# Optimization experiments

Measured on AMD Instinct MI355X. Metric: run time of the kernel, lower is better.

## Reference

```python
import jax, jax.numpy as jnp
import numpy as np

N_NODES = 100000
N_EDGES = 800000
D_IN = 128
D_H = 512


def _glorot(key, shape):
    fan_in, fan_out = shape[1], shape[0]
    lim = jnp.sqrt(6.0 / (fan_in + fan_out))
    return jax.random.uniform(key, shape, jnp.float32, -lim, lim)


def setup_inputs() -> dict:
    key = jax.random.key(0)
    ks = jax.random.split(key, 16)
    x = jax.random.normal(ks[0], (N_NODES, D_IN), jnp.float32)
    edge_index = jax.random.randint(ks[1], (2, N_EDGES), 0, N_NODES, jnp.int64)
    return {
        "x": x,
        "edge_index": edge_index,
        # SAGEConv layer1: lin_l (neighbors, with bias), lin_r (root, no bias)
        "Wl1": _glorot(ks[2], (D_H, D_IN)), "bl1": jnp.zeros((D_H,), jnp.float32),
        "Wr1": _glorot(ks[3], (D_H, D_IN)),
        # SAGEConv layer2
        "Wl2": _glorot(ks[4], (D_H, D_H)), "bl2": jnp.zeros((D_H,), jnp.float32),
        "Wr2": _glorot(ks[5], (D_H, D_H)),
        # SAGEConv layer3
        "Wl3": _glorot(ks[6], (D_H, D_H)), "bl3": jnp.zeros((D_H,), jnp.float32),
        "Wr3": _glorot(ks[7], (D_H, D_H)),
        # residual projections W, W2 (nn.Linear with bias)
        "Ww": _glorot(ks[8], (D_H, D_IN)), "bw": jnp.zeros((D_H,), jnp.float32),
        "Ww2": _glorot(ks[9], (D_H, D_IN)), "bw2": jnp.zeros((D_H,), jnp.float32),
        # shared PReLU parameter (nn.PReLU default: single param init 0.25)
        "a": jnp.array(0.25, jnp.float32),
    }


def _prelu(x, a):
    return jnp.where(x > 0, x, a * x)


def _sage_conv(x, src, dst, Wl, bl, Wr):
    # mean-aggregate neighbor features x[src] onto dst, then linear + root term
    msg = jax.ops.segment_sum(x[src], dst, num_segments=N_NODES)  # [N, d]
    deg = jax.ops.segment_sum(jnp.ones((src.shape[0],), x.dtype), dst,
                              num_segments=N_NODES)
    agg = msg / jnp.maximum(deg, 1.0)[:, None]
    return agg @ Wl.T + bl + x @ Wr.T


def reference(x, edge_index, Wl1, bl1, Wr1, Wl2, bl2, Wr2, Wl3, bl3, Wr3,
              Ww, bw, Ww2, bw2, a):
    src, dst = edge_index[0], edge_index[1]
    h1 = _prelu(_sage_conv(x, src, dst, Wl1, bl1, Wr1), a)
    h2 = _prelu(_sage_conv(h1 + (x @ Ww.T + bw), src, dst, Wl2, bl2, Wr2), a)
    h3 = _prelu(_sage_conv(h2 + h1 + (x @ Ww2.T + bw2), src, dst, Wl3, bl3, Wr3), a)
    return h3
```

## Files before the change

kernel.cpp:

```cpp
#include <hip/hip_runtime.h>
#include <stddef.h>

#define NN 100000
#define NE 800000
#define DIN 128
#define DH 512
#define MT 782

typedef __attribute__((ext_vector_type(8))) short sh8;
typedef __attribute__((ext_vector_type(4))) float f32x4;

__device__ __forceinline__ unsigned short f2b(float f) {
  unsigned u = __float_as_uint(f);
  return (unsigned short)((u + 0x7FFFu + ((u >> 16) & 1u)) >> 16);
}
__device__ __forceinline__ float b2f(unsigned short s) {
  return __uint_as_float(((unsigned)s) << 16);
}

__device__ __forceinline__ void gload16(const unsigned short* g, unsigned short* l) {
  __builtin_amdgcn_global_load_lds(
      (const __attribute__((address_space(1))) void*)g,
      (__attribute__((address_space(3))) void*)l, 16, 0, 0);
}


__global__ void k_count(const int* __restrict__ dst, int* __restrict__ cnt) {
  int i = blockIdx.x * blockDim.x + threadIdx.x;
  if (i < NE) atomicAdd(&cnt[dst[i]], 1);
}

__global__ void k_invdeg(const int* __restrict__ cnt, float* __restrict__ inv_deg) {
  int i = blockIdx.x * blockDim.x + threadIdx.x;
  if (i < NN) inv_deg[i] = 1.0f / (float)(cnt[i] > 1 ? cnt[i] : 1);
}

__global__ void k_scan1(const int* __restrict__ cnt, int* __restrict__ excl,
                        int* __restrict__ partials) {
  __shared__ int sh[256];
  int tid = threadIdx.x;
  int base = blockIdx.x * 1024 + tid * 4;
  int v[4]; int s = 0;
#pragma unroll
  for (int i = 0; i < 4; i++) { int idx = base + i; v[i] = (idx < NN) ? cnt[idx] : 0; s += v[i]; }
  sh[tid] = s; __syncthreads();
  for (int off = 1; off < 256; off <<= 1) {
    int t = (tid >= off) ? sh[tid - off] : 0;
    __syncthreads();
    sh[tid] += t;
    __syncthreads();
  }
  int run = sh[tid] - s;
#pragma unroll
  for (int i = 0; i < 4; i++) { int idx = base + i; if (idx < NN) excl[idx] = run; run += v[i]; }
  if (tid == 255) partials[blockIdx.x] = sh[255];
}

__global__ void k_scan2(int* __restrict__ partials, int* __restrict__ row_start, int nparts) {
  __shared__ int sh[128];
  int tid = threadIdx.x;
  int v = (tid < nparts) ? partials[tid] : 0;
  sh[tid] = v; __syncthreads();
  for (int off = 1; off < 128; off <<= 1) {
    int t = (tid >= off) ? sh[tid - off] : 0;
    __syncthreads();
    sh[tid] += t;
    __syncthreads();
  }
  if (tid < nparts) partials[tid] = sh[tid] - v;
  if (tid == 127) row_start[NN] = sh[127];
}

__global__ void k_scan3(int* __restrict__ excl, const int* __restrict__ partials) {
  int i = blockIdx.x * blockDim.x + threadIdx.x;
  if (i < NN) excl[i] += partials[i >> 10];
}

__global__ void k_fill(const int* __restrict__ src, const int* __restrict__ dst,
                       const int* __restrict__ row_start, int* __restrict__ cursor,
                       int* __restrict__ ssrc) {
  int i = blockIdx.x * blockDim.x + threadIdx.x;
  if (i < NE) {
    int d = dst[i];
    int pos = atomicAdd(&cursor[d], 1);
    ssrc[row_start[d] + pos] = src[i];
  }
}


__global__ void k_f2b(const float* __restrict__ src, unsigned short* __restrict__ dst, int n) {
  int i = (blockIdx.x * blockDim.x + threadIdx.x) * 4;
  if (i < n) {
    float4 v = *(const float4*)(src + i);
    ushort4 o;
    o.x = f2b(v.x); o.y = f2b(v.y); o.z = f2b(v.z); o.w = f2b(v.w);
    *(ushort4*)(dst + i) = o;
  }
}


__global__ __launch_bounds__(256) void k_aggb512(
    const unsigned short* __restrict__ z, const int* __restrict__ rs,
    const int* __restrict__ ssrc, const float* __restrict__ inv_deg,
    unsigned short* __restrict__ agg) {
  int w = (blockIdx.x * blockDim.x + threadIdx.x) >> 6;
  int lane = threadIdx.x & 63;
  if (w >= NN) return;
  int e0 = rs[w], e1 = rs[w + 1];
  float acc[8] = {0, 0, 0, 0, 0, 0, 0, 0};
  for (int e = e0; e < e1; ++e) {
    int s = ssrc[e];
    sh8 v = *(const sh8*)(z + (size_t)s * DH + lane * 8);
#pragma unroll
    for (int j = 0; j < 8; ++j) acc[j] += b2f((unsigned short)v[j]);
  }
  float s0 = inv_deg[w];
  sh8 o;
#pragma unroll
  for (int j = 0; j < 8; ++j) o[j] = (short)f2b(acc[j] * s0);
  *(sh8*)(agg + (size_t)w * DH + lane * 8) = o;
}

__global__ __launch_bounds__(256) void k_aggb128(
    const unsigned short* __restrict__ z, const int* __restrict__ rs,
    const int* __restrict__ ssrc, const float* __restrict__ inv_deg,
    unsigned short* __restrict__ agg) {
  int w = (blockIdx.x * blockDim.x + threadIdx.x) >> 6;
  int lane = threadIdx.x & 63;
  if (w >= NN) return;
  int e0 = rs[w], e1 = rs[w + 1];
  float a0 = 0.f, a1 = 0.f;
  for (int e = e0; e < e1; ++e) {
    int s = ssrc[e];
    unsigned v = *(const unsigned*)(z + (size_t)s * DIN + lane * 2);
    a0 += b2f((unsigned short)(v & 0xFFFFu));
    a1 += b2f((unsigned short)(v >> 16));
  }
  float s0 = inv_deg[w];
  unsigned o = (unsigned)f2b(a0 * s0) | ((unsigned)f2b(a1 * s0) << 16);
  *(unsigned*)(agg + (size_t)w * DIN + lane * 2) = o;
}


__device__ __forceinline__ void stage_tile(
    unsigned short* ldsA, unsigned short* ldsB,
    const unsigned short* __restrict__ A, int sA, int m0,
    const unsigned short* __restrict__ B, int sB, int n0,
    int k0, int tid) {
  const int w = tid >> 6, l = tid & 63;
  const int kc = (l & 3) * 8;
  const int rsub = l >> 2;
#pragma unroll
  for (int i = 0; i < 2; ++i) {
    int rl = w * 32 + i * 16 + rsub;
    int ra = m0 + rl; if (ra >= NN) ra = NN - 1;
    gload16(A + (size_t)ra * sA + k0 + kc, ldsA + (size_t)(w * 32 + i * 16) * 32);
    gload16(B + (size_t)(n0 + rl) * sB + k0 + kc, ldsB + (size_t)(w * 32 + i * 16) * 32);
  }
}

__device__ __forceinline__ void mfma_step(
    const unsigned short* As, const unsigned short* Bs,
    int wr, int wc, int r16, int kg, f32x4 (&acc)[4][4]) {
  sh8 af[4], bf[4];
#pragma unroll
  for (int i = 0; i < 4; ++i)
    af[i] = *(const sh8*)&As[(wr + i * 16 + r16) * 32 + kg * 8];
#pragma unroll
  for (int j = 0; j < 4; ++j)
    bf[j] = *(const sh8*)&Bs[(wc + j * 16 + r16) * 32 + kg * 8];
#pragma unroll
  for (int i = 0; i < 4; ++i)
#pragma unroll
    for (int j = 0; j < 4; ++j)
      acc[i][j] = __builtin_amdgcn_mfma_f32_16x16x32_bf16(af[i], bf[j], acc[i][j], 0, 0, 0);
}

__global__ __launch_bounds__(256, 2) void k_gemm1(
    const unsigned short* __restrict__ ag, const unsigned short* __restrict__ xb,
    const unsigned short* __restrict__ Wl1, const unsigned short* __restrict__ Wr1,
    const unsigned short* __restrict__ Ww, const unsigned short* __restrict__ Ww2,
    const float* __restrict__ bl1, const float* __restrict__ bw,
    const float* __restrict__ bw2, const float* __restrict__ aptr,
    unsigned short* __restrict__ z2o, unsigned short* __restrict__ z3po) {
  __shared__ __align__(16) unsigned short As[128 * 32];
  __shared__ __align__(16) unsigned short Bs[128 * 32];
  const int tid = threadIdx.x;
  const int m0 = blockIdx.x * 128, n0 = blockIdx.y * 128;
  const int wid = tid >> 6, lane = tid & 63;
  const int r16 = lane & 15, kg = lane >> 4;
  const int wr = (wid >> 1) * 64, wc = (wid & 1) * 64;

  f32x4 a0[4][4], a1[4][4], a2[4][4];
#pragma unroll
  for (int i = 0; i < 4; ++i)
#pragma unroll
    for (int j = 0; j < 4; ++j) { a0[i][j] = 0.f; a1[i][j] = 0.f; a2[i][j] = 0.f; }

  for (int s = 0; s < 16; ++s) {
    const int seg = s >> 2, k0 = (s & 3) * 32;
    const unsigned short* Ap = (seg == 0) ? ag : xb;
    const unsigned short* Bp = (seg == 0) ? Wl1 : (seg == 1) ? Wr1 : (seg == 2) ? Ww : Ww2;
    stage_tile(As, Bs, Ap, DIN, m0, Bp, DIN, n0, k0, tid);
    __syncthreads();
    if (seg <= 1)      mfma_step(As, Bs, wr, wc, r16, kg, a0);
    else if (seg == 2) mfma_step(As, Bs, wr, wc, r16, kg, a1);
    else               mfma_step(As, Bs, wr, wc, r16, kg, a2);
    __syncthreads();
  }

  const float aval = aptr[0];
#pragma unroll
  for (int i = 0; i < 4; ++i) {
    const int mbase = m0 + wr + i * 16 + kg * 4;
#pragma unroll
    for (int j = 0; j < 4; ++j) {
      const int col = n0 + wc + j * 16 + r16;
      const float b1 = bl1[col], b2 = bw[col], b3 = bw2[col];
#pragma unroll
      for (int r = 0; r < 4; ++r) {
        const int m = mbase + r;
        if (m >= NN) continue;
        float h1 = a0[i][j][r] + b1;
        h1 = h1 > 0.f ? h1 : aval * h1;
        z2o[(size_t)m * DH + col] = f2b(h1 + a1[i][j][r] + b2);
        z3po[(size_t)m * DH + col] = f2b(h1 + a2[i][j][r] + b3);
      }
    }
  }
}

template <bool LAST>
__global__ __launch_bounds__(256, 4) void k_gemm23(
    const unsigned short* __restrict__ Aag, const unsigned short* __restrict__ Az,
    const unsigned short* __restrict__ Wl, const unsigned short* __restrict__ Wr,
    const float* __restrict__ bl, const float* __restrict__ aptr,
    const unsigned short* __restrict__ z3p, void* __restrict__ outp) {
  __shared__ __align__(16) unsigned short As[128 * 32];
  __shared__ __align__(16) unsigned short Bs[128 * 32];
  const int tid = threadIdx.x;
  const int m0 = blockIdx.x * 128, n0 = blockIdx.y * 128;
  const int wid = tid >> 6, lane = tid & 63;
  const int r16 = lane & 15, kg = lane >> 4;
  const int wr = (wid >> 1) * 64, wc = (wid & 1) * 64;

  f32x4 acc[4][4];
#pragma unroll
  for (int i = 0; i < 4; ++i)
#pragma unroll
    for (int j = 0; j < 4; ++j) acc[i][j] = 0.f;

  for (int s = 0; s < 32; ++s) {
    const int k0 = (s & 15) * 32;
    const unsigned short* Ap = (s < 16) ? Aag : Az;
    const unsigned short* Bp = (s < 16) ? Wl : Wr;
    stage_tile(As, Bs, Ap, DH, m0, Bp, DH, n0, k0, tid);
    __syncthreads();
    mfma_step(As, Bs, wr, wc, r16, kg, acc);
    __syncthreads();
  }

  const float aval = aptr[0];
  float* outf = (float*)outp;
  unsigned short* outb = (unsigned short*)outp;
#pragma unroll
  for (int i = 0; i < 4; ++i) {
    const int mbase = m0 + wr + i * 16 + kg * 4;
#pragma unroll
    for (int j = 0; j < 4; ++j) {
      const int col = n0 + wc + j * 16 + r16;
      const float bv = bl[col];
#pragma unroll
      for (int r = 0; r < 4; ++r) {
        const int m = mbase + r;
        if (m >= NN) continue;
        float h = acc[i][j][r] + bv;
        h = h > 0.f ? h : aval * h;
        if constexpr (LAST) {
          outf[(size_t)m * DH + col] = h;
        } else {
          outb[(size_t)m * DH + col] = f2b(h + b2f(z3p[(size_t)m * DH + col]));
        }
      }
    }
  }
}


extern "C" void kernel_launch(void* const* d_in, const int* in_sizes, int n_in,
                              void* d_out, int out_size, void* d_ws, size_t ws_size,
                              hipStream_t stream) {
  const float* x = (const float*)d_in[0];
  const int* ei = (const int*)d_in[1];
  const float* Wl1 = (const float*)d_in[2];
  const float* bl1 = (const float*)d_in[3];
  const float* Wr1 = (const float*)d_in[4];
  const float* Wl2 = (const float*)d_in[5];
  const float* bl2 = (const float*)d_in[6];
  const float* Wr2 = (const float*)d_in[7];
  const float* Wl3 = (const float*)d_in[8];
  const float* bl3 = (const float*)d_in[9];
  const float* Wr3 = (const float*)d_in[10];
  const float* Ww  = (const float*)d_in[11];
  const float* bw  = (const float*)d_in[12];
  const float* Ww2 = (const float*)d_in[13];
  const float* bw2 = (const float*)d_in[14];
  const float* ap  = (const float*)d_in[15];
  float* out = (float*)d_out;

  const size_t MP = 100096;
  char* w = (char*)d_ws;
  size_t off = 0;
  unsigned short* xb   = (unsigned short*)(w + off); off += MP * DIN * 2;
  unsigned short* ag1  = (unsigned short*)(w + off); off += MP * DIN * 2;
  unsigned short* agb  = (unsigned short*)(w + off); off += MP * DH * 2;
  unsigned short* zb   = (unsigned short*)(w + off); off += MP * DH * 2;
  unsigned short* zc   = (unsigned short*)(w + off); off += MP * DH * 2;
  unsigned short* z3pb = (unsigned short*)(w + off); off += MP * DH * 2;
  unsigned short* Wl1b = (unsigned short*)(w + off); off += (size_t)DH * DIN * 2;
  unsigned short* Wr1b = (unsigned short*)(w + off); off += (size_t)DH * DIN * 2;
  unsigned short* Wwb  = (unsigned short*)(w + off); off += (size_t)DH * DIN * 2;
  unsigned short* Ww2b = (unsigned short*)(w + off); off += (size_t)DH * DIN * 2;
  unsigned short* Wl2b = (unsigned short*)(w + off); off += (size_t)DH * DH * 2;
  unsigned short* Wr2b = (unsigned short*)(w + off); off += (size_t)DH * DH * 2;
  unsigned short* Wl3b = (unsigned short*)(w + off); off += (size_t)DH * DH * 2;
  unsigned short* Wr3b = (unsigned short*)(w + off); off += (size_t)DH * DH * 2;
  float* inv_deg = (float*)(w + off); off += (size_t)NN * 4;
  int* row_start = (int*)(w + off); off += (size_t)(NN + 1) * 4;
  int* cursor = (int*)(w + off); off += (size_t)NN * 4;
  int* ssrc = (int*)(w + off); off += (size_t)NE * 4;
  int* partials = (int*)(w + off); off += 512;

  const int* esrc = ei;
  const int* edst = ei + NE;

  hipMemsetAsync(cursor, 0, NN * 4, stream);
  k_count<<<(NE + 255) / 256, 256, 0, stream>>>(edst, cursor);
  k_invdeg<<<(NN + 255) / 256, 256, 0, stream>>>(cursor, inv_deg);
  k_scan1<<<(NN + 1023) / 1024, 256, 0, stream>>>(cursor, row_start, partials);
  k_scan2<<<1, 128, 0, stream>>>(partials, row_start, (NN + 1023) / 1024);
  k_scan3<<<(NN + 255) / 256, 256, 0, stream>>>(row_start, partials);
  hipMemsetAsync(cursor, 0, NN * 4, stream);
  k_fill<<<(NE + 255) / 256, 256, 0, stream>>>(esrc, edst, row_start, cursor, ssrc);

  const int WK = DH * DIN;
  const int WB = DH * DH;
  k_f2b<<<(WK / 4 + 255) / 256, 256, 0, stream>>>(Wl1, Wl1b, WK);
  k_f2b<<<(WK / 4 + 255) / 256, 256, 0, stream>>>(Wr1, Wr1b, WK);
  k_f2b<<<(WK / 4 + 255) / 256, 256, 0, stream>>>(Ww,  Wwb,  WK);
  k_f2b<<<(WK / 4 + 255) / 256, 256, 0, stream>>>(Ww2, Ww2b, WK);
  k_f2b<<<(WB / 4 + 255) / 256, 256, 0, stream>>>(Wl2, Wl2b, WB);
  k_f2b<<<(WB / 4 + 255) / 256, 256, 0, stream>>>(Wr2, Wr2b, WB);
  k_f2b<<<(WB / 4 + 255) / 256, 256, 0, stream>>>(Wl3, Wl3b, WB);
  k_f2b<<<(WB / 4 + 255) / 256, 256, 0, stream>>>(Wr3, Wr3b, WB);
  k_f2b<<<(NN * DIN / 4 + 255) / 256, 256, 0, stream>>>(x, xb, NN * DIN);

  dim3 gg(MT, 4);

  k_aggb128<<<(NN + 3) / 4, 256, 0, stream>>>(xb, row_start, ssrc, inv_deg, ag1);
  k_gemm1<<<gg, 256, 0, stream>>>(ag1, xb, Wl1b, Wr1b, Wwb, Ww2b, bl1, bw, bw2, ap,
                                  zb, z3pb);
  k_aggb512<<<(NN + 3) / 4, 256, 0, stream>>>(zb, row_start, ssrc, inv_deg, agb);
  k_gemm23<false><<<gg, 256, 0, stream>>>(agb, zb, Wl2b, Wr2b, bl2, ap, z3pb, zc);
  k_aggb512<<<(NN + 3) / 4, 256, 0, stream>>>(zc, row_start, ssrc, inv_deg, agb);
  k_gemm23<true><<<gg, 256, 0, stream>>>(agb, zc, Wl3b, Wr3b, bl3, ap, nullptr, out);
}
```

Measured before the change: 1.066 ms.

## Replace LDS-staged GEMMs with direct-to-register MFMA and unroll aggregation loops

The GEMM kernels drop LDS staging and barriers. Each wave now loads A and B fragments straight from global memory into registers with double buffering. Each block spans the full 512-column output with 8 waves, so a block reads its rows of A once instead of four times across column tiles. The risks are redundant global loads of A across waves (only the L2/L1 cache helps), uncoalesced fragment loads, and higher register pressure from the 8x4 accumulators. The neighbor aggregation loops also process two edges per iteration to raise memory-level parallelism.

Measured after the change: 1.642 ms. +54.1%, slower.

```diff
diff --git a/kernel.cpp b/kernel.cpp
--- a/kernel.cpp
+++ b/kernel.cpp
@@ -5,7 +5,6 @@
 #define NE 800000
 #define DIN 128
 #define DH 512
-#define MT 782
 
 typedef __attribute__((ext_vector_type(8))) short sh8;
 typedef __attribute__((ext_vector_type(4))) float f32x4;
@@ -16,12 +15,6 @@
 }
 __device__ __forceinline__ float b2f(unsigned short s) {
   return __uint_as_float(((unsigned)s) << 16);
-}
-
-__device__ __forceinline__ void gload16(const unsigned short* g, unsigned short* l) {
-  __builtin_amdgcn_global_load_lds(
-      (const __attribute__((address_space(1))) void*)g,
-      (__attribute__((address_space(3))) void*)l, 16, 0, 0);
 }
 
 
@@ -108,11 +101,19 @@
   if (w >= NN) return;
   int e0 = rs[w], e1 = rs[w + 1];
   float acc[8] = {0, 0, 0, 0, 0, 0, 0, 0};
-  for (int e = e0; e < e1; ++e) {
-    int s = ssrc[e];
-    sh8 v = *(const sh8*)(z + (size_t)s * DH + lane * 8);
-#pragma unroll
-    for (int j = 0; j < 8; ++j) acc[j] += b2f((unsigned short)v[j]);
+  int e = e0;
+  for (; e + 1 < e1; e += 2) {
+    int sa = ssrc[e], sb = ssrc[e + 1];
+    sh8 va = *(const sh8*)(z + (size_t)sa * DH + lane * 8);
+    sh8 vb = *(const sh8*)(z + (size_t)sb * DH + lane * 8);
+#pragma unroll
+    for (int j = 0; j < 8; ++j) acc[j] += b2f((unsigned short)va[j]) + b2f((unsigned short)vb[j]);
+  }
+  if (e < e1) {
+    int sa = ssrc[e];
+    sh8 va = *(const sh8*)(z + (size_t)sa * DH + lane * 8);
+#pragma unroll
+    for (int j = 0; j < 8; ++j) acc[j] += b2f((unsigned short)va[j]);
   }
   float s0 = inv_deg[w];
   sh8 o;
@@ -130,11 +131,18 @@
   if (w >= NN) return;
   int e0 = rs[w], e1 = rs[w + 1];
   float a0 = 0.f, a1 = 0.f;
-  for (int e = e0; e < e1; ++e) {
-    int s = ssrc[e];
-    unsigned v = *(const unsigned*)(z + (size_t)s * DIN + lane * 2);
-    a0 += b2f((unsigned short)(v & 0xFFFFu));
-    a1 += b2f((unsigned short)(v >> 16));
+  int e = e0;
+  for (; e + 1 < e1; e += 2) {
+    int sa = ssrc[e], sb = ssrc[e + 1];
+    unsigned va = *(const unsigned*)(z + (size_t)sa * DIN + lane * 2);
+    unsigned vb = *(const unsigned*)(z + (size_t)sb * DIN + lane * 2);
+    a0 += b2f((unsigned short)(va & 0xFFFFu)) + b2f((unsigned short)(vb & 0xFFFFu));
+    a1 += b2f((unsigned short)(va >> 16)) + b2f((unsigned short)(vb >> 16));
+  }
+  if (e < e1) {
+    unsigned va = *(const unsigned*)(z + (size_t)ssrc[e] * DIN + lane * 2);
+    a0 += b2f((unsigned short)(va & 0xFFFFu));
+    a1 += b2f((unsigned short)(va >> 16));
   }
   float s0 = inv_deg[w];
   unsigned o = (unsigned)f2b(a0 * s0) | ((unsigned)f2b(a1 * s0) << 16);
@@ -142,54 +150,97 @@
 }
 
 
-__device__ __forceinline__ void stage_tile(
-    unsigned short* ldsA, unsigned short* ldsB,
-    const unsigned short* __restrict__ A, int sA, int m0,
-    const unsigned short* __restrict__ B, int sB, int n0,
-    int k0, int tid) {
-  const int w = tid >> 6, l = tid & 63;
-  const int kc = (l & 3) * 8;
-  const int rsub = l >> 2;
-#pragma unroll
-  for (int i = 0; i < 2; ++i) {
-    int rl = w * 32 + i * 16 + rsub;
-    int ra = m0 + rl; if (ra >= NN) ra = NN - 1;
-    gload16(A + (size_t)ra * sA + k0 + kc, ldsA + (size_t)(w * 32 + i * 16) * 32);
-    gload16(B + (size_t)(n0 + rl) * sB + k0 + kc, ldsB + (size_t)(w * 32 + i * 16) * 32);
-  }
-}
-
-__device__ __forceinline__ void mfma_step(
-    const unsigned short* As, const unsigned short* Bs,
-    int wr, int wc, int r16, int kg, f32x4 (&acc)[4][4]) {
-  sh8 af[4], bf[4];
-#pragma unroll
-  for (int i = 0; i < 4; ++i)
-    af[i] = *(const sh8*)&As[(wr + i * 16 + r16) * 32 + kg * 8];
-#pragma unroll
-  for (int j = 0; j < 4; ++j)
-    bf[j] = *(const sh8*)&Bs[(wc + j * 16 + r16) * 32 + kg * 8];
-#pragma unroll
-  for (int i = 0; i < 4; ++i)
-#pragma unroll
-    for (int j = 0; j < 4; ++j)
-      acc[i][j] = __builtin_amdgcn_mfma_f32_16x16x32_bf16(af[i], bf[j], acc[i][j], 0, 0, 0);
-}
-
-__global__ __launch_bounds__(256, 2) void k_gemm1(
+__device__ __forceinline__ void ng_half512(
+    const unsigned short* __restrict__ A, const int* arow,
+    const unsigned short* __restrict__ W, const int* brow,
+    int ko, f32x4 (&acc)[8][4]) {
+  sh8 Af[2][8], Bf[2][4];
+#pragma unroll
+  for (int i = 0; i < 8; ++i) Af[0][i] = *(const sh8*)(A + (size_t)arow[i] * DH + ko);
+#pragma unroll
+  for (int j = 0; j < 4; ++j) Bf[0][j] = *(const sh8*)(W + (size_t)brow[j] * DH + ko);
+#pragma unroll
+  for (int s = 0; s < 16; s += 2) {
+    const int k1 = (s + 1) * 32 + ko;
+#pragma unroll
+    for (int i = 0; i < 8; ++i) Af[1][i] = *(const sh8*)(A + (size_t)arow[i] * DH + k1);
+#pragma unroll
+    for (int j = 0; j < 4; ++j) Bf[1][j] = *(const sh8*)(W + (size_t)brow[j] * DH + k1);
+#pragma unroll
+    for (int i = 0; i < 8; ++i)
+#pragma unroll
+      for (int j = 0; j < 4; ++j)
+        acc[i][j] = __builtin_amdgcn_mfma_f32_16x16x32_bf16(Af[0][i], Bf[0][j], acc[i][j], 0, 0, 0);
+    if (s + 2 < 16) {
+      const int k2 = (s + 2) * 32 + ko;
+#pragma unroll
+      for (int i = 0; i < 8; ++i) Af[0][i] = *(const sh8*)(A + (size_t)arow[i] * DH + k2);
+#pragma unroll
+      for (int j = 0; j < 4; ++j) Bf[0][j] = *(const sh8*)(W + (size_t)brow[j] * DH + k2);
+    }
+#pragma unroll
+    for (int i = 0; i < 8; ++i)
+#pragma unroll
+      for (int j = 0; j < 4; ++j)
+        acc[i][j] = __builtin_amdgcn_mfma_f32_16x16x32_bf16(Af[1][i], Bf[1][j], acc[i][j], 0, 0, 0);
+  }
+}
+
+__device__ __forceinline__ void ng_q128(
+    const unsigned short* __restrict__ A, const int* arow,
+    const unsigned short* __restrict__ W, const int* brow,
+    int ko, f32x4 (&acc)[4][4]) {
+  sh8 Af[2][4], Bf[2][4];
+#pragma unroll
+  for (int i = 0; i < 4; ++i) Af[0][i] = *(const sh8*)(A + (size_t)arow[i] * DIN + ko);
+#pragma unroll
+  for (int j = 0; j < 4; ++j) Bf[0][j] = *(const sh8*)(W + (size_t)brow[j] * DIN + ko);
+#pragma unroll
+  for (int s = 0; s < 4; s += 2) {
+    const int k1 = (s + 1) * 32 + ko;
+#pragma unroll
+    for (int i = 0; i < 4; ++i) Af[1][i] = *(const sh8*)(A + (size_t)arow[i] * DIN + k1);
+#pragma unroll
+    for (int j = 0; j < 4; ++j) Bf[1][j] = *(const sh8*)(W + (size_t)brow[j] * DIN + k1);
+#pragma unroll
+    for (int i = 0; i < 4; ++i)
+#pragma unroll
+      for (int j = 0; j < 4; ++j)
+        acc[i][j] = __builtin_amdgcn_mfma_f32_16x16x32_bf16(Af[0][i], Bf[0][j], acc[i][j], 0, 0, 0);
+    if (s + 2 < 4) {
+      const int k2 = (s + 2) * 32 + ko;
+#pragma unroll
+      for (int i = 0; i < 4; ++i) Af[0][i] = *(const sh8*)(A + (size_t)arow[i] * DIN + k2);
+#pragma unroll
+      for (int j = 0; j < 4; ++j) Bf[0][j] = *(const sh8*)(W + (size_t)brow[j] * DIN + k2);
+    }
+#pragma unroll
+    for (int i = 0; i < 4; ++i)
+#pragma unroll
+      for (int j = 0; j < 4; ++j)
+        acc[i][j] = __builtin_amdgcn_mfma_f32_16x16x32_bf16(Af[1][i], Bf[1][j], acc[i][j], 0, 0, 0);
+  }
+}
+
+__global__ __launch_bounds__(512) void k_ng1(
     const unsigned short* __restrict__ ag, const unsigned short* __restrict__ xb,
     const unsigned short* __restrict__ Wl1, const unsigned short* __restrict__ Wr1,
     const unsigned short* __restrict__ Ww, const unsigned short* __restrict__ Ww2,
     const float* __restrict__ bl1, const float* __restrict__ bw,
     const float* __restrict__ bw2, const float* __restrict__ aptr,
     unsigned short* __restrict__ z2o, unsigned short* __restrict__ z3po) {
-  __shared__ __align__(16) unsigned short As[128 * 32];
-  __shared__ __align__(16) unsigned short Bs[128 * 32];
-  const int tid = threadIdx.x;
-  const int m0 = blockIdx.x * 128, n0 = blockIdx.y * 128;
-  const int wid = tid >> 6, lane = tid & 63;
-  const int r16 = lane & 15, kg = lane >> 4;
-  const int wr = (wid >> 1) * 64, wc = (wid & 1) * 64;
+  const int m0 = blockIdx.x * 64;
+  const int l = threadIdx.x & 63, w = threadIdx.x >> 6;
+  const int r16 = l & 15, kg = l >> 4;
+  const int n0w = w * 64;
+  const int ko = kg * 8;
+
+  int arow[4], brow[4];
+#pragma unroll
+  for (int i = 0; i < 4; ++i) {
+    int r = m0 + i * 16 + r16; arow[i] = r < NN ? r : NN - 1;
+    brow[i] = n0w + i * 16 + r16;
+  }
 
   f32x4 a0[4][4], a1[4][4], a2[4][4];
 #pragma unroll
@@ -197,25 +248,18 @@
 #pragma unroll
     for (int j = 0; j < 4; ++j) { a0[i][j] = 0.f; a1[i][j] = 0.f; a2[i][j] = 0.f; }
 
-  for (int s = 0; s < 16; ++s) {
-    const int seg = s >> 2, k0 = (s & 3) * 32;
-    const unsigned short* Ap = (seg == 0) ? ag : xb;
-    const unsigned short* Bp = (seg == 0) ? Wl1 : (seg == 1) ? Wr1 : (seg == 2) ? Ww : Ww2;
-    stage_tile(As, Bs, Ap, DIN, m0, Bp, DIN, n0, k0, tid);
-    __syncthreads();
-    if (seg <= 1)      mfma_step(As, Bs, wr, wc, r16, kg, a0);
-    else if (seg == 2) mfma_step(As, Bs, wr, wc, r16, kg, a1);
-    else               mfma_step(As, Bs, wr, wc, r16, kg, a2);
-    __syncthreads();
-  }
+  ng_q128(ag, arow, Wl1, brow, ko, a0);
+  ng_q128(xb, arow, Wr1, brow, ko, a0);
+  ng_q128(xb, arow, Ww,  brow, ko, a1);
+  ng_q128(xb, arow, Ww2, brow, ko, a2);
 
   const float aval = aptr[0];
 #pragma unroll
   for (int i = 0; i < 4; ++i) {
-    const int mbase = m0 + wr + i * 16 + kg * 4;
+    const int mbase = m0 + i * 16 + kg * 4;
 #pragma unroll
     for (int j = 0; j < 4; ++j) {
-      const int col = n0 + wc + j * 16 + r16;
+      const int col = n0w + j * 16 + r16;
       const float b1 = bl1[col], b2 = bw[col], b3 = bw2[col];
 #pragma unroll
       for (int r = 0; r < 4; ++r) {
@@ -231,44 +275,41 @@
 }
 
 template <bool LAST>
-__global__ __launch_bounds__(256, 4) void k_gemm23(
+__global__ __launch_bounds__(512) void k_ng23(
     const unsigned short* __restrict__ Aag, const unsigned short* __restrict__ Az,
     const unsigned short* __restrict__ Wl, const unsigned short* __restrict__ Wr,
     const float* __restrict__ bl, const float* __restrict__ aptr,
     const unsigned short* __restrict__ z3p, void* __restrict__ outp) {
-  __shared__ __align__(16) unsigned short As[128 * 32];
-  __shared__ __align__(16) unsigned short Bs[128 * 32];
-  const int tid = threadIdx.x;
-  const int m0 = blockIdx.x * 128, n0 = blockIdx.y * 128;
-  const int wid = tid >> 6, lane = tid & 63;
-  const int r16 = lane & 15, kg = lane >> 4;
-  const int wr = (wid >> 1) * 64, wc = (wid & 1) * 64;
-
-  f32x4 acc[4][4];
-#pragma unroll
-  for (int i = 0; i < 4; ++i)
+  const int m0 = blockIdx.x * 128;
+  const int l = threadIdx.x & 63, w = threadIdx.x >> 6;
+  const int r16 = l & 15, kg = l >> 4;
+  const int n0w = w * 64;
+  const int ko = kg * 8;
+
+  int arow[8], brow[4];
+#pragma unroll
+  for (int i = 0; i < 8; ++i) { int r = m0 + i * 16 + r16; arow[i] = r < NN ? r : NN - 1; }
+#pragma unroll
+  for (int j = 0; j < 4; ++j) brow[j] = n0w + j * 16 + r16;
+
+  f32x4 acc[8][4];
+#pragma unroll
+  for (int i = 0; i < 8; ++i)
 #pragma unroll
     for (int j = 0; j < 4; ++j) acc[i][j] = 0.f;
 
-  for (int s = 0; s < 32; ++s) {
-    const int k0 = (s & 15) * 32;
-    const unsigned short* Ap = (s < 16) ? Aag : Az;
-    const unsigned short* Bp = (s < 16) ? Wl : Wr;
-    stage_tile(As, Bs, Ap, DH, m0, Bp, DH, n0, k0, tid);
-    __syncthreads();
-    mfma_step(As, Bs, wr, wc, r16, kg, acc);
-    __syncthreads();
-  }
+  ng_half512(Aag, arow, Wl, brow, ko, acc);
+  ng_half512(Az,  arow, Wr, brow, ko, acc);
 
   const float aval = aptr[0];
   float* outf = (float*)outp;
   unsigned short* outb = (unsigned short*)outp;
 #pragma unroll
-  for (int i = 0; i < 4; ++i) {
-    const int mbase = m0 + wr + i * 16 + kg * 4;
+  for (int i = 0; i < 8; ++i) {
+    const int mbase = m0 + i * 16 + kg * 4;
 #pragma unroll
     for (int j = 0; j < 4; ++j) {
-      const int col = n0 + wc + j * 16 + r16;
+      const int col = n0w + j * 16 + r16;
       const float bv = bl[col];
 #pragma unroll
       for (int r = 0; r < 4; ++r) {
@@ -355,13 +396,11 @@
   k_f2b<<<(WB / 4 + 255) / 256, 256, 0, stream>>>(Wr3, Wr3b, WB);
   k_f2b<<<(NN * DIN / 4 + 255) / 256, 256, 0, stream>>>(x, xb, NN * DIN);
 
-  dim3 gg(MT, 4);
-
   k_aggb128<<<(NN + 3) / 4, 256, 0, stream>>>(xb, row_start, ssrc, inv_deg, ag1);
-  k_gemm1<<<gg, 256, 0, stream>>>(ag1, xb, Wl1b, Wr1b, Wwb, Ww2b, bl1, bw, bw2, ap,
+  k_ng1<<<1564, 512, 0, stream>>>(ag1, xb, Wl1b, Wr1b, Wwb, Ww2b, bl1, bw, bw2, ap,
                                   zb, z3pb);
   k_aggb512<<<(NN + 3) / 4, 256, 0, stream>>>(zb, row_start, ssrc, inv_deg, agb);
-  k_gemm23<false><<<gg, 256, 0, stream>>>(agb, zb, Wl2b, Wr2b, bl2, ap, z3pb, zc);
+  k_ng23<false><<<782, 512, 0, stream>>>(agb, zb, Wl2b, Wr2b, bl2, ap, z3pb, zc);
   k_aggb512<<<(NN + 3) / 4, 256, 0, stream>>>(zc, row_start, ssrc, inv_deg, agb);
-  k_gemm23<true><<<gg, 256, 0, stream>>>(agb, zc, Wl3b, Wr3b, bl3, ap, nullptr, out);
-}
+  k_ng23<true><<<782, 512, 0, stream>>>(agb, zc, Wl3b, Wr3b, bl3, ap, nullptr, out);
+}
```
